# Performance work log

Measured on AMD Instinct MI355X. Metric: run time of the kernel, lower is better.

The kernel has to match this reference:

```python
import jax, jax.numpy as jnp
import numpy as np

B, N_POINTS, LATENT, K = 16384, 4096, 64, 1024
COMMIT = 0.25


def _init_linear(key, fan_in, fan_out):
    kw, kb = jax.random.split(key)
    w = jax.random.normal(kw, (fan_in, fan_out), jnp.float32) / jnp.sqrt(jnp.float32(fan_in))
    b = jnp.zeros((fan_out,), jnp.float32)
    return w, b


def setup_inputs() -> dict:
    key = jax.random.key(0)
    ks = jax.random.split(key, 8)
    x = jax.random.normal(ks[0], (B, N_POINTS), jnp.float32)
    enc_w1, enc_b1 = _init_linear(ks[1], N_POINTS, 512)
    enc_w2, enc_b2 = _init_linear(ks[2], 512, 256)
    enc_w3, enc_b3 = _init_linear(ks[3], 256, LATENT)
    # codebook init uniform(-1/K, 1/K) like the torch code
    codebook = jax.random.uniform(ks[4], (K, LATENT), jnp.float32, -1.0 / K, 1.0 / K)
    dec_w1, dec_b1 = _init_linear(ks[5], LATENT, 256)
    dec_w2, dec_b2 = _init_linear(ks[6], 256, 512)
    dec_w3, dec_b3 = _init_linear(ks[7], 512, N_POINTS)
    return {"x": x,
            "enc_w1": enc_w1, "enc_b1": enc_b1, "enc_w2": enc_w2, "enc_b2": enc_b2,
            "enc_w3": enc_w3, "enc_b3": enc_b3, "codebook": codebook,
            "dec_w1": dec_w1, "dec_b1": dec_b1, "dec_w2": dec_w2, "dec_b2": dec_b2,
            "dec_w3": dec_w3, "dec_b3": dec_b3}


def reference(x, enc_w1, enc_b1, enc_w2, enc_b2, enc_w3, enc_b3, codebook,
              dec_w1, dec_b1, dec_w2, dec_b2, dec_w3, dec_b3):
    # encoder MLP: N_POINTS -> 512 -> 256 -> LATENT
    h = jax.nn.relu(x @ enc_w1 + enc_b1)
    h = jax.nn.relu(h @ enc_w2 + enc_b2)
    z = h @ enc_w3 + enc_b3                       # [B, LATENT]
    # vector quantization: squared distances to codebook, argmin, gather
    d = (jnp.sum(z * z, axis=1, keepdims=True)
         - 2.0 * z @ codebook.T
         + jnp.sum(codebook * codebook, axis=1))  # [B, K]
    idx = jnp.argmin(d, axis=1)                   # [B]
    zq = codebook[idx]                            # [B, LATENT]
    vq_loss = (jnp.mean((jax.lax.stop_gradient(zq) - z) ** 2)
               + COMMIT * jnp.mean((zq - jax.lax.stop_gradient(z)) ** 2))
    zq_st = z + jax.lax.stop_gradient(zq - z)     # straight-through
    # decoder MLP: LATENT -> 256 -> 512 -> N_POINTS
    h = jax.nn.relu(zq_st @ dec_w1 + dec_b1)
    h = jax.nn.relu(h @ dec_w2 + dec_b2)
    xh = h @ dec_w3 + dec_b3                      # [B, N_POINTS]
    recon_loss = jnp.mean((xh - x) ** 2)
    total_loss = recon_loss + vq_loss
    return xh, idx, total_loss, recon_loss, vq_loss
```

## Files before the change

### kernel.cpp

```cpp
#include <hip/hip_runtime.h>

#define B_    16384
#define NPTS  4096
#define LAT   64
#define KCB   1024

template<bool RELU, bool FUSE_LOSS>
__global__ __launch_bounds__(256)
void gemm128_kernel(const float* __restrict__ A, const float* __restrict__ W,
                    const float* __restrict__ bias, float* __restrict__ C,
                    int M, int N, int Kd,
                    const float* __restrict__ X, float* __restrict__ loss_acc)
{
    constexpr int BM = 128, BN = 128, BK = 16;
    __shared__ __align__(16) float As[BK][BM + 4];
    __shared__ __align__(16) float Bs[BK][BN + 4];

    const int tid = threadIdx.x;
    const int tx = tid & 15;
    const int ty = tid >> 4;
    const int m0 = blockIdx.y * BM;
    const int n0 = blockIdx.x * BN;

    float acc[2][2][4][4] = {};

    for (int k0 = 0; k0 < Kd; k0 += BK) {
        #pragma unroll
        for (int h = 0; h < 2; ++h) {
            const int f  = tid + h * 256;
            const int r  = f >> 2;
            const int c4 = f & 3;
            const float4 a4 = *(const float4*)(A + (size_t)(m0 + r) * Kd + k0 + c4 * 4);
            As[c4 * 4 + 0][r] = a4.x;
            As[c4 * 4 + 1][r] = a4.y;
            As[c4 * 4 + 2][r] = a4.z;
            As[c4 * 4 + 3][r] = a4.w;
        }
        #pragma unroll
        for (int h = 0; h < 2; ++h) {
            const int f = tid + h * 256;
            const int r = f >> 5;
            const int c = f & 31;
            const float4 b4 = *(const float4*)(W + (size_t)(k0 + r) * N + n0 + c * 4);
            *(float4*)&Bs[r][c * 4] = b4;
        }
        __syncthreads();

        #pragma unroll
        for (int kk = 0; kk < BK; ++kk) {
            float a[2][4], b[2][4];
            #pragma unroll
            for (int rh = 0; rh < 2; ++rh) {
                const float4 v = *(const float4*)&As[kk][rh * 64 + ty * 4];
                a[rh][0] = v.x; a[rh][1] = v.y; a[rh][2] = v.z; a[rh][3] = v.w;
            }
            #pragma unroll
            for (int ch = 0; ch < 2; ++ch) {
                const float4 v = *(const float4*)&Bs[kk][ch * 64 + tx * 4];
                b[ch][0] = v.x; b[ch][1] = v.y; b[ch][2] = v.z; b[ch][3] = v.w;
            }
            #pragma unroll
            for (int rh = 0; rh < 2; ++rh)
                #pragma unroll
                for (int i = 0; i < 4; ++i)
                    #pragma unroll
                    for (int ch = 0; ch < 2; ++ch)
                        #pragma unroll
                        for (int j = 0; j < 4; ++j)
                            acc[rh][ch][i][j] += a[rh][i] * b[ch][j];
        }
        __syncthreads();
    }

    float4 bv[2];
    #pragma unroll
    for (int ch = 0; ch < 2; ++ch)
        bv[ch] = *(const float4*)(bias + n0 + ch * 64 + tx * 4);

    float lsum = 0.f;
    #pragma unroll
    for (int rh = 0; rh < 2; ++rh) {
        #pragma unroll
        for (int i = 0; i < 4; ++i) {
            const int m = m0 + rh * 64 + ty * 4 + i;
            float* crow = C + (size_t)m * N;
            #pragma unroll
            for (int ch = 0; ch < 2; ++ch) {
                const int n = n0 + ch * 64 + tx * 4;
                float4 o;
                o.x = acc[rh][ch][i][0] + bv[ch].x;
                o.y = acc[rh][ch][i][1] + bv[ch].y;
                o.z = acc[rh][ch][i][2] + bv[ch].z;
                o.w = acc[rh][ch][i][3] + bv[ch].w;
                if (RELU) {
                    o.x = fmaxf(o.x, 0.f); o.y = fmaxf(o.y, 0.f);
                    o.z = fmaxf(o.z, 0.f); o.w = fmaxf(o.w, 0.f);
                }
                if (FUSE_LOSS) {
                    const float4 xv = *(const float4*)(X + (size_t)m * N + n);
                    const float d0 = o.x - xv.x, d1 = o.y - xv.y;
                    const float d2 = o.z - xv.z, d3 = o.w - xv.w;
                    lsum += d0 * d0 + d1 * d1 + d2 * d2 + d3 * d3;
                }
                *(float4*)(crow + n) = o;
            }
        }
    }

    if (FUSE_LOSS) {
        __shared__ float red[256];
        red[tid] = lsum;
        __syncthreads();
        for (int s = 128; s > 0; s >>= 1) {
            if (tid < s) red[tid] += red[tid + s];
            __syncthreads();
        }
        if (tid == 0) atomicAdd(loss_acc, red[0]);
    }
}

template<bool RELU, bool FUSE_LOSS>
__global__ __launch_bounds__(256)
void gemm_kernel(const float* __restrict__ A, const float* __restrict__ W,
                 const float* __restrict__ bias, float* __restrict__ C,
                 int M, int N, int Kd,
                 const float* __restrict__ X, float* __restrict__ loss_acc)
{
    const int BM = 64, BN = 64, BK = 16;
    __shared__ float As[BK][BM + 4];
    __shared__ float Bs[BK][BN + 4];

    const int tid = threadIdx.x;
    const int tx = tid & 15;
    const int ty = tid >> 4;
    const int m0 = blockIdx.y * BM;
    const int n0 = blockIdx.x * BN;

    float acc[4][4] = {};

    for (int k0 = 0; k0 < Kd; k0 += BK) {
        {
            const int r  = tid >> 2;
            const int c4 = tid & 3;
            const float4 a4 = *(const float4*)(A + (size_t)(m0 + r) * Kd + k0 + c4 * 4);
            As[c4 * 4 + 0][r] = a4.x;
            As[c4 * 4 + 1][r] = a4.y;
            As[c4 * 4 + 2][r] = a4.z;
            As[c4 * 4 + 3][r] = a4.w;
        }
        {
            const int r  = tid >> 4;
            const int c4 = tid & 15;
            const float4 b4 = *(const float4*)(W + (size_t)(k0 + r) * N + n0 + c4 * 4);
            *(float4*)&Bs[r][c4 * 4] = b4;
        }
        __syncthreads();

        #pragma unroll
        for (int kk = 0; kk < BK; ++kk) {
            const float4 a4 = *(const float4*)&As[kk][ty * 4];
            const float4 b4 = *(const float4*)&Bs[kk][tx * 4];
            const float av[4] = {a4.x, a4.y, a4.z, a4.w};
            const float bv[4] = {b4.x, b4.y, b4.z, b4.w};
            #pragma unroll
            for (int i = 0; i < 4; ++i)
                #pragma unroll
                for (int j = 0; j < 4; ++j)
                    acc[i][j] += av[i] * bv[j];
        }
        __syncthreads();
    }

    float lsum = 0.f;
    #pragma unroll
    for (int i = 0; i < 4; ++i) {
        const int m = m0 + ty * 4 + i;
        #pragma unroll
        for (int j = 0; j < 4; ++j) {
            const int n = n0 + tx * 4 + j;
            float v = acc[i][j] + bias[n];
            if (RELU) v = fmaxf(v, 0.f);
            C[(size_t)m * N + n] = v;
            if (FUSE_LOSS) {
                const float d = v - X[(size_t)m * N + n];
                lsum += d * d;
            }
        }
    }

    if (FUSE_LOSS) {
        __shared__ float red[256];
        red[tid] = lsum;
        __syncthreads();
        for (int s = 128; s > 0; s >>= 1) {
            if (tid < s) red[tid] += red[tid + s];
            __syncthreads();
        }
        if (tid == 0) atomicAdd(loss_acc, red[0]);
    }
}

__global__ __launch_bounds__(256)
void cbnorm_kernel(const float* __restrict__ cb, float* __restrict__ sc)
{
    const int c = blockIdx.x * blockDim.x + threadIdx.x;
    if (c < KCB) {
        double s = 0.0;
        #pragma unroll 16
        for (int j = 0; j < LAT; ++j) {
            const float v = cb[(size_t)c * LAT + j];
            s += (double)v * (double)v;
        }
        sc[c] = (float)s;
    }
}

#define VQROWS 4
__global__ __launch_bounds__(256)
void vq_assign_kernel(const float* __restrict__ z, const float* __restrict__ cb,
                      const float* __restrict__ sc, float* __restrict__ zq,
                      float* __restrict__ idx_out)
{
    __shared__ float zrow[VQROWS][LAT];
    __shared__ float sS[VQROWS];
    __shared__ float rd[256];
    __shared__ int   ri[256];

    const int row0 = blockIdx.x * VQROWS;
    const int tid = threadIdx.x;

    zrow[tid >> 6][tid & 63] = z[(size_t)row0 * LAT + tid];
    __syncthreads();
    if (tid < VQROWS) {
        double s = 0.0;
        for (int j = 0; j < LAT; ++j) s += (double)zrow[tid][j] * (double)zrow[tid][j];
        sS[tid] = (float)s;
    }
    __syncthreads();

    float bestd[VQROWS];
    int   besti[VQROWS];
    #pragma unroll
    for (int r = 0; r < VQROWS; ++r) { bestd[r] = 1e30f; besti[r] = KCB; }

    for (int c = tid; c < KCB; c += 256) {
        const float4* cb4 = (const float4*)(cb + (size_t)c * LAT);
        double dot[VQROWS] = {};
        #pragma unroll
        for (int q = 0; q < LAT / 4; ++q) {
            const float4 cv = cb4[q];
            #pragma unroll
            for (int r = 0; r < VQROWS; ++r) {
                const float4 zv = ((const float4*)zrow[r])[q];
                dot[r] += (double)zv.x * cv.x + (double)zv.y * cv.y
                        + (double)zv.z * cv.z + (double)zv.w * cv.w;
            }
        }
        #pragma unroll
        for (int r = 0; r < VQROWS; ++r) {
            const float zc = (float)dot[r];
            const float d  = (sS[r] - 2.0f * zc) + sc[c];
            if (d < bestd[r] || (d == bestd[r] && c < besti[r])) {
                bestd[r] = d; besti[r] = c;
            }
        }
    }

    for (int r = 0; r < VQROWS; ++r) {
        rd[tid] = bestd[r]; ri[tid] = besti[r];
        __syncthreads();
        for (int s = 128; s > 0; s >>= 1) {
            if (tid < s) {
                const float od = rd[tid + s];
                const int   oi = ri[tid + s];
                if (od < rd[tid] || (od == rd[tid] && oi < ri[tid])) {
                    rd[tid] = od; ri[tid] = oi;
                }
            }
            __syncthreads();
        }
        const int best = ri[0];
        if (tid == 0) idx_out[row0 + r] = (float)best;
        if (tid < LAT) zq[(size_t)(row0 + r) * LAT + tid] = cb[(size_t)best * LAT + tid];
        __syncthreads();
    }
}

__global__ __launch_bounds__(256)
void vq_loss_kernel(const float* __restrict__ z, const float* __restrict__ zq,
                    float* __restrict__ acc, int n)
{
    float s = 0.f;
    for (int i = blockIdx.x * blockDim.x + threadIdx.x; i < n;
         i += gridDim.x * blockDim.x) {
        const float d = zq[i] - z[i];
        s += d * d;
    }
    __shared__ float red[256];
    red[threadIdx.x] = s;
    __syncthreads();
    for (int t = 128; t > 0; t >>= 1) {
        if (threadIdx.x < t) red[threadIdx.x] += red[threadIdx.x + t];
        __syncthreads();
    }
    if (threadIdx.x == 0) atomicAdd(acc, red[0]);
}

__global__ void finalize_kernel(const float* __restrict__ acc, float* __restrict__ out3)
{
    const float recon = acc[0] / ((float)B_ * (float)NPTS);
    const float vq    = 1.25f * (acc[1] / ((float)B_ * (float)LAT));
    out3[0] = recon + vq;
    out3[1] = recon;
    out3[2] = vq;
}

extern "C" void kernel_launch(void* const* d_in, const int* in_sizes, int n_in,
                              void* d_out, int out_size, void* d_ws, size_t ws_size,
                              hipStream_t stream)
{
    const float* x   = (const float*)d_in[0];
    const float* ew1 = (const float*)d_in[1];
    const float* eb1 = (const float*)d_in[2];
    const float* ew2 = (const float*)d_in[3];
    const float* eb2 = (const float*)d_in[4];
    const float* ew3 = (const float*)d_in[5];
    const float* eb3 = (const float*)d_in[6];
    const float* cb  = (const float*)d_in[7];
    const float* dw1 = (const float*)d_in[8];
    const float* db1 = (const float*)d_in[9];
    const float* dw2 = (const float*)d_in[10];
    const float* db2 = (const float*)d_in[11];
    const float* dw3 = (const float*)d_in[12];
    const float* db3 = (const float*)d_in[13];

    float* out_xh     = (float*)d_out;
    float* out_idx    = out_xh + (size_t)B_ * NPTS;
    float* out_losses = out_idx + B_;

    float* ws   = (float*)d_ws;
    float* bufA = ws;
    float* bufB = bufA + (size_t)B_ * 512;
    float* z    = bufB + (size_t)B_ * 256;
    float* zq   = z + (size_t)B_ * LAT;
    float* sc   = zq + (size_t)B_ * LAT;
    float* acc  = sc + KCB;

    hipMemsetAsync(acc, 0, 2 * sizeof(float), stream);

    const dim3 blk(256);

    gemm128_kernel<true,  false><<<dim3(512 / 128, B_ / 128), blk, 0, stream>>>(
        x, ew1, eb1, bufA, B_, 512, NPTS, nullptr, nullptr);
    gemm128_kernel<true,  false><<<dim3(256 / 128, B_ / 128), blk, 0, stream>>>(
        bufA, ew2, eb2, bufB, B_, 256, 512, nullptr, nullptr);
    gemm_kernel<false, false><<<dim3(64 / 64,  B_ / 64), blk, 0, stream>>>(
        bufB, ew3, eb3, z, B_, 64, 256, nullptr, nullptr);

    cbnorm_kernel<<<dim3(KCB / 256), blk, 0, stream>>>(cb, sc);
    vq_assign_kernel<<<dim3(B_ / VQROWS), blk, 0, stream>>>(z, cb, sc, zq, out_idx);
    vq_loss_kernel<<<dim3(256), blk, 0, stream>>>(z, zq, acc + 1, B_ * LAT);

    gemm_kernel<true,  false><<<dim3(256 / 64, B_ / 64), blk, 0, stream>>>(
        zq, dw1, db1, bufB, B_, 256, LAT, nullptr, nullptr);
    gemm128_kernel<true,  false><<<dim3(512 / 128, B_ / 128), blk, 0, stream>>>(
        bufB, dw2, db2, bufA, B_, 512, 256, nullptr, nullptr);
    gemm128_kernel<false, true ><<<dim3(NPTS / 128, B_ / 128), blk, 0, stream>>>(
        bufA, dw3, db3, out_xh, B_, NPTS, 512, x, acc + 0);

    finalize_kernel<<<1, 1, 0, stream>>>(acc, out_losses);
}
```

Before: 2.598 ms.

## Run decoder output GEMM on bf16 MFMA with hi/lo split precision

The final decoder GEMM (512->4096, the largest) moves from an FP32 SIMT tiled kernel to bf16 MFMA 16x16x32 instructions. Both activations and weights are split into bf16 high and low parts, and three MFMA products approximate FP32 accuracy. The previous GEMM now writes the split activations directly, and a new kernel pre-transposes and splits dec_w3 on every call. The change also doubles BK in gemm128 and moves the second encoder layer to the 64x64 kernel. The costs are three MFMA passes, twice the operand traffic, and slightly reduced precision from dropping the lo*lo term.

```diff
diff --git a/kernel.cpp b/kernel.cpp
--- a/kernel.cpp
+++ b/kernel.cpp
@@ -5,14 +5,26 @@
 #define LAT   64
 #define KCB   1024
 
-template<bool RELU, bool FUSE_LOSS>
+typedef __attribute__((ext_vector_type(8))) short bf16x8;
+typedef __attribute__((ext_vector_type(4))) float f32x4;
+
+__device__ inline unsigned short f2bf(float x) {
+    union { float f; unsigned u; } v; v.f = x;
+    unsigned r = v.u + 0x7fffu + ((v.u >> 16) & 1u);
+    return (unsigned short)(r >> 16);
+}
+__device__ inline float bf2f(unsigned short h) {
+    union { unsigned u; float f; } v; v.u = ((unsigned)h) << 16;
+    return v.f;
+}
+
+template<bool RELU>
 __global__ __launch_bounds__(256)
 void gemm128_kernel(const float* __restrict__ A, const float* __restrict__ W,
                     const float* __restrict__ bias, float* __restrict__ C,
-                    int M, int N, int Kd,
-                    const float* __restrict__ X, float* __restrict__ loss_acc)
-{
-    constexpr int BM = 128, BN = 128, BK = 16;
+                    int M, int N, int Kd)
+{
+    constexpr int BM = 128, BN = 128, BK = 32;
     __shared__ __align__(16) float As[BK][BM + 4];
     __shared__ __align__(16) float Bs[BK][BN + 4];
 
@@ -26,10 +38,10 @@
 
     for (int k0 = 0; k0 < Kd; k0 += BK) {
         #pragma unroll
-        for (int h = 0; h < 2; ++h) {
+        for (int h = 0; h < 4; ++h) {
             const int f  = tid + h * 256;
-            const int r  = f >> 2;
-            const int c4 = f & 3;
+            const int r  = f >> 3;
+            const int c4 = f & 7;
             const float4 a4 = *(const float4*)(A + (size_t)(m0 + r) * Kd + k0 + c4 * 4);
             As[c4 * 4 + 0][r] = a4.x;
             As[c4 * 4 + 1][r] = a4.y;
@@ -37,7 +49,7 @@
             As[c4 * 4 + 3][r] = a4.w;
         }
         #pragma unroll
-        for (int h = 0; h < 2; ++h) {
+        for (int h = 0; h < 4; ++h) {
             const int f = tid + h * 256;
             const int r = f >> 5;
             const int c = f & 31;
@@ -77,7 +89,6 @@
     for (int ch = 0; ch < 2; ++ch)
         bv[ch] = *(const float4*)(bias + n0 + ch * 64 + tx * 4);
 
-    float lsum = 0.f;
     #pragma unroll
     for (int rh = 0; rh < 2; ++rh) {
         #pragma unroll
@@ -96,35 +107,18 @@
                     o.x = fmaxf(o.x, 0.f); o.y = fmaxf(o.y, 0.f);
                     o.z = fmaxf(o.z, 0.f); o.w = fmaxf(o.w, 0.f);
                 }
-                if (FUSE_LOSS) {
-                    const float4 xv = *(const float4*)(X + (size_t)m * N + n);
-                    const float d0 = o.x - xv.x, d1 = o.y - xv.y;
-                    const float d2 = o.z - xv.z, d3 = o.w - xv.w;
-                    lsum += d0 * d0 + d1 * d1 + d2 * d2 + d3 * d3;
-                }
                 *(float4*)(crow + n) = o;
             }
         }
     }
-
-    if (FUSE_LOSS) {
-        __shared__ float red[256];
-        red[tid] = lsum;
-        __syncthreads();
-        for (int s = 128; s > 0; s >>= 1) {
-            if (tid < s) red[tid] += red[tid + s];
-            __syncthreads();
-        }
-        if (tid == 0) atomicAdd(loss_acc, red[0]);
-    }
-}
-
-template<bool RELU, bool FUSE_LOSS>
+}
+
+template<bool RELU, bool SPLIT_OUT>
 __global__ __launch_bounds__(256)
 void gemm_kernel(const float* __restrict__ A, const float* __restrict__ W,
                  const float* __restrict__ bias, float* __restrict__ C,
                  int M, int N, int Kd,
-                 const float* __restrict__ X, float* __restrict__ loss_acc)
+                 unsigned short* __restrict__ Ohi, unsigned short* __restrict__ Olo)
 {
     const int BM = 64, BN = 64, BK = 16;
     __shared__ float As[BK][BM + 4];
@@ -171,33 +165,164 @@
         __syncthreads();
     }
 
-    float lsum = 0.f;
     #pragma unroll
     for (int i = 0; i < 4; ++i) {
         const int m = m0 + ty * 4 + i;
+        const int n = n0 + tx * 4;
+        float v[4];
         #pragma unroll
         for (int j = 0; j < 4; ++j) {
-            const int n = n0 + tx * 4 + j;
-            float v = acc[i][j] + bias[n];
-            if (RELU) v = fmaxf(v, 0.f);
-            C[(size_t)m * N + n] = v;
-            if (FUSE_LOSS) {
-                const float d = v - X[(size_t)m * N + n];
+            v[j] = acc[i][j] + bias[n + j];
+            if (RELU) v[j] = fmaxf(v[j], 0.f);
+        }
+        if (SPLIT_OUT) {
+            ushort4 h4, l4;
+            unsigned short* hp = (unsigned short*)&h4;
+            unsigned short* lp = (unsigned short*)&l4;
+            #pragma unroll
+            for (int j = 0; j < 4; ++j) {
+                const unsigned short hi = f2bf(v[j]);
+                hp[j] = hi;
+                lp[j] = f2bf(v[j] - bf2f(hi));
+            }
+            *(ushort4*)&Ohi[(size_t)m * N + n] = h4;
+            *(ushort4*)&Olo[(size_t)m * N + n] = l4;
+        } else {
+            float4 o; o.x = v[0]; o.y = v[1]; o.z = v[2]; o.w = v[3];
+            *(float4*)&C[(size_t)m * N + n] = o;
+        }
+    }
+}
+
+__global__ __launch_bounds__(256)
+void split_w3t_kernel(const float* __restrict__ Win,
+                      unsigned short* __restrict__ Whi,
+                      unsigned short* __restrict__ Wlo)
+{
+    __shared__ float t[64][65];
+    const int tid = threadIdx.x;
+    const int tx = tid & 63;
+    const int ty = tid >> 6;
+    const int n0 = blockIdx.x * 64;
+    const int k0 = blockIdx.y * 64;
+
+    #pragma unroll
+    for (int i = 0; i < 16; ++i) {
+        const int kk = ty + i * 4;
+        t[kk][tx] = Win[(size_t)(k0 + kk) * NPTS + n0 + tx];
+    }
+    __syncthreads();
+    #pragma unroll
+    for (int i = 0; i < 16; ++i) {
+        const int nn = ty + i * 4;
+        const float v = t[tx][nn];
+        const unsigned short hi = f2bf(v);
+        const size_t off = (size_t)(n0 + nn) * 512 + k0 + tx;
+        Whi[off] = hi;
+        Wlo[off] = f2bf(v - bf2f(hi));
+    }
+}
+
+__global__ __launch_bounds__(256)
+void mfma_dec3_kernel(const unsigned short* __restrict__ Ah,
+                      const unsigned short* __restrict__ Al,
+                      const unsigned short* __restrict__ Wh,
+                      const unsigned short* __restrict__ Wl,
+                      const float* __restrict__ bias,
+                      float* __restrict__ C,
+                      const float* __restrict__ X,
+                      float* __restrict__ loss_acc)
+{
+    constexpr int K = 512, N = NPTS;
+    constexpr int BM = 128, BN = 128, BK = 32;
+    __shared__ __align__(16) unsigned short sAh[BM][BK];
+    __shared__ __align__(16) unsigned short sAl[BM][BK];
+    __shared__ __align__(16) unsigned short sBh[BN][BK];
+    __shared__ __align__(16) unsigned short sBl[BN][BK];
+
+    const int tid = threadIdx.x;
+    const int w  = tid >> 6;
+    const int l  = tid & 63;
+    const int wr = w >> 1, wc = w & 1;
+    const int lr = l & 15;
+    const int lk = l >> 4;
+    const int m0 = blockIdx.y * BM;
+    const int n0 = blockIdx.x * BN;
+
+    f32x4 acc[4][4];
+    const f32x4 zero4 = {0.f, 0.f, 0.f, 0.f};
+    #pragma unroll
+    for (int i = 0; i < 4; ++i)
+        #pragma unroll
+        for (int j = 0; j < 4; ++j) acc[i][j] = zero4;
+
+    const int r0 = tid >> 2,        kp0 = (tid & 3) * 8;
+    const int r1 = (tid + 256) >> 2, kp1 = (tid & 3) * 8;
+
+    for (int k0 = 0; k0 < K; k0 += BK) {
+        const uint4 vah0 = *(const uint4*)(Ah + (size_t)(m0 + r0) * K + k0 + kp0);
+        const uint4 vah1 = *(const uint4*)(Ah + (size_t)(m0 + r1) * K + k0 + kp1);
+        const uint4 val0 = *(const uint4*)(Al + (size_t)(m0 + r0) * K + k0 + kp0);
+        const uint4 val1 = *(const uint4*)(Al + (size_t)(m0 + r1) * K + k0 + kp1);
+        const uint4 vbh0 = *(const uint4*)(Wh + (size_t)(n0 + r0) * K + k0 + kp0);
+        const uint4 vbh1 = *(const uint4*)(Wh + (size_t)(n0 + r1) * K + k0 + kp1);
+        const uint4 vbl0 = *(const uint4*)(Wl + (size_t)(n0 + r0) * K + k0 + kp0);
+        const uint4 vbl1 = *(const uint4*)(Wl + (size_t)(n0 + r1) * K + k0 + kp1);
+        __syncthreads();
+        *(uint4*)&sAh[r0][kp0] = vah0;  *(uint4*)&sAh[r1][kp1] = vah1;
+        *(uint4*)&sAl[r0][kp0] = val0;  *(uint4*)&sAl[r1][kp1] = val1;
+        *(uint4*)&sBh[r0][kp0] = vbh0;  *(uint4*)&sBh[r1][kp1] = vbh1;
+        *(uint4*)&sBl[r0][kp0] = vbl0;  *(uint4*)&sBl[r1][kp1] = vbl1;
+        __syncthreads();
+
+        bf16x8 fah[4], fal[4], fbh[4], fbl[4];
+        #pragma unroll
+        for (int r = 0; r < 4; ++r) {
+            fah[r] = *(const bf16x8*)&sAh[wr * 64 + r * 16 + lr][lk * 8];
+            fal[r] = *(const bf16x8*)&sAl[wr * 64 + r * 16 + lr][lk * 8];
+        }
+        #pragma unroll
+        for (int c = 0; c < 4; ++c) {
+            fbh[c] = *(const bf16x8*)&sBh[wc * 64 + c * 16 + lr][lk * 8];
+            fbl[c] = *(const bf16x8*)&sBl[wc * 64 + c * 16 + lr][lk * 8];
+        }
+        #pragma unroll
+        for (int r = 0; r < 4; ++r)
+            #pragma unroll
+            for (int c = 0; c < 4; ++c) {
+                acc[r][c] = __builtin_amdgcn_mfma_f32_16x16x32_bf16(fah[r], fbh[c], acc[r][c], 0, 0, 0);
+                acc[r][c] = __builtin_amdgcn_mfma_f32_16x16x32_bf16(fah[r], fbl[c], acc[r][c], 0, 0, 0);
+                acc[r][c] = __builtin_amdgcn_mfma_f32_16x16x32_bf16(fal[r], fbh[c], acc[r][c], 0, 0, 0);
+            }
+    }
+
+    float lsum = 0.f;
+    #pragma unroll
+    for (int c = 0; c < 4; ++c) {
+        const int col = n0 + wc * 64 + c * 16 + lr;
+        const float bv = bias[col];
+        #pragma unroll
+        for (int r = 0; r < 4; ++r) {
+            const int rowb = m0 + wr * 64 + r * 16 + lk * 4;
+            #pragma unroll
+            for (int q = 0; q < 4; ++q) {
+                const float v = acc[r][c][q] + bv;
+                const size_t off = (size_t)(rowb + q) * N + col;
+                const float d = v - X[off];
                 lsum += d * d;
-            }
-        }
-    }
-
-    if (FUSE_LOSS) {
-        __shared__ float red[256];
-        red[tid] = lsum;
-        __syncthreads();
-        for (int s = 128; s > 0; s >>= 1) {
-            if (tid < s) red[tid] += red[tid + s];
-            __syncthreads();
-        }
-        if (tid == 0) atomicAdd(loss_acc, red[0]);
-    }
+                C[off] = v;
+            }
+        }
+    }
+
+    __shared__ float red[256];
+    red[tid] = lsum;
+    __syncthreads();
+    for (int s = 128; s > 0; s >>= 1) {
+        if (tid < s) red[tid] += red[tid + s];
+        __syncthreads();
+    }
+    if (tid == 0) atomicAdd(loss_acc, red[0]);
 }
 
 __global__ __launch_bounds__(256)
@@ -345,28 +470,34 @@
     float* zq   = z + (size_t)B_ * LAT;
     float* sc   = zq + (size_t)B_ * LAT;
     float* acc  = sc + KCB;
+    unsigned short* wt3hi = (unsigned short*)(acc + 16);
+    unsigned short* wt3lo = wt3hi + (size_t)NPTS * 512;
+    unsigned short* h4hi  = (unsigned short*)bufA;
+    unsigned short* h4lo  = h4hi + (size_t)B_ * 512;
 
     hipMemsetAsync(acc, 0, 2 * sizeof(float), stream);
 
     const dim3 blk(256);
 
-    gemm128_kernel<true,  false><<<dim3(512 / 128, B_ / 128), blk, 0, stream>>>(
-        x, ew1, eb1, bufA, B_, 512, NPTS, nullptr, nullptr);
-    gemm128_kernel<true,  false><<<dim3(256 / 128, B_ / 128), blk, 0, stream>>>(
+    split_w3t_kernel<<<dim3(NPTS / 64, 512 / 64), blk, 0, stream>>>(dw3, wt3hi, wt3lo);
+
+    gemm128_kernel<true><<<dim3(512 / 128, B_ / 128), blk, 0, stream>>>(
+        x, ew1, eb1, bufA, B_, 512, NPTS);
+    gemm_kernel<true, false><<<dim3(256 / 64, B_ / 64), blk, 0, stream>>>(
         bufA, ew2, eb2, bufB, B_, 256, 512, nullptr, nullptr);
-    gemm_kernel<false, false><<<dim3(64 / 64,  B_ / 64), blk, 0, stream>>>(
+    gemm_kernel<false, false><<<dim3(64 / 64, B_ / 64), blk, 0, stream>>>(
         bufB, ew3, eb3, z, B_, 64, 256, nullptr, nullptr);
 
     cbnorm_kernel<<<dim3(KCB / 256), blk, 0, stream>>>(cb, sc);
     vq_assign_kernel<<<dim3(B_ / VQROWS), blk, 0, stream>>>(z, cb, sc, zq, out_idx);
     vq_loss_kernel<<<dim3(256), blk, 0, stream>>>(z, zq, acc + 1, B_ * LAT);
 
-    gemm_kernel<true,  false><<<dim3(256 / 64, B_ / 64), blk, 0, stream>>>(
+    gemm_kernel<true, false><<<dim3(256 / 64, B_ / 64), blk, 0, stream>>>(
         zq, dw1, db1, bufB, B_, 256, LAT, nullptr, nullptr);
-    gemm128_kernel<true,  false><<<dim3(512 / 128, B_ / 128), blk, 0, stream>>>(
-        bufB, dw2, db2, bufA, B_, 512, 256, nullptr, nullptr);
-    gemm128_kernel<false, true ><<<dim3(NPTS / 128, B_ / 128), blk, 0, stream>>>(
-        bufA, dw3, db3, out_xh, B_, NPTS, 512, x, acc + 0);
+    gemm_kernel<true, true><<<dim3(512 / 64, B_ / 64), blk, 0, stream>>>(
+        bufB, dw2, db2, nullptr, B_, 512, 256, h4hi, h4lo);
+    mfma_dec3_kernel<<<dim3(NPTS / 128, B_ / 128), blk, 0, stream>>>(
+        h4hi, h4lo, wt3hi, wt3lo, db3, out_xh, x, acc + 0);
 
     finalize_kernel<<<1, 1, 0, stream>>>(acc, out_losses);
 }
```

New measurement: 2.177 ms. -16.2%, faster.
